# Kernel optimization log

Hardware: AMD Instinct MI355X
Metric: run time of the kernel (lower is better)

Reference implementation:

```python
import jax, jax.numpy as jnp
import numpy as np
from jax import lax

B, T, F_IN = 8, 512, 229
C1 = 48            # model_size_conv // 16
C3 = 96            # model_size_conv // 8
D_CONV = 768       # model_size_conv
D_LSTM = 768       # model_size_lstm
N_PITCH = 88       # MAX_MIDI - MIN_MIDI + 1
N_STATE = 5
EMB = 2
LSTM_IN = D_CONV + N_PITCH * EMB   # 944
FC_IN = C3 * (F_IN // 4)           # 96 * 57 = 5472
BN_EPS = 1e-5


def setup_inputs() -> dict:
    key = jax.random.key(0)
    ks = iter(jax.random.split(key, 64))
    nrm = lambda shape, s=0.05: jax.random.normal(next(ks), shape, jnp.float32) * s
    uni = lambda shape: jax.random.uniform(next(ks), shape, jnp.float32, 0.5, 1.5)
    inp = {
        'mel': jax.random.normal(next(ks), (B, T, F_IN), jnp.float32),
        'conv1_w': nrm((C1, 1, 3, 3)), 'conv1_b': nrm((C1,)),
        'bn1_g': uni((C1,)), 'bn1_b': nrm((C1,)), 'bn1_m': nrm((C1,), 0.1), 'bn1_v': uni((C1,)),
        'conv2_w': nrm((C1, C1, 3, 3)), 'conv2_b': nrm((C1,)),
        'bn2_g': uni((C1,)), 'bn2_b': nrm((C1,)), 'bn2_m': nrm((C1,), 0.1), 'bn2_v': uni((C1,)),
        'conv3_w': nrm((C3, C1, 3, 3)), 'conv3_b': nrm((C3,)),
        'bn3_g': uni((C3,)), 'bn3_b': nrm((C3,)), 'bn3_m': nrm((C3,), 0.1), 'bn3_v': uni((C3,)),
        'fc_w': nrm((D_CONV, FC_IN)), 'fc_b': nrm((D_CONV,)),
        'wih1': nrm((4 * D_LSTM, LSTM_IN)), 'whh1': nrm((4 * D_LSTM, D_LSTM)),
        'bih1': nrm((4 * D_LSTM,)), 'bhh1': nrm((4 * D_LSTM,)),
        'wih2': nrm((4 * D_LSTM, D_LSTM)), 'whh2': nrm((4 * D_LSTM, D_LSTM)),
        'bih2': nrm((4 * D_LSTM,)), 'bhh2': nrm((4 * D_LSTM,)),
        'post_w': nrm((N_PITCH * N_STATE, D_LSTM)), 'post_b': nrm((N_PITCH * N_STATE,)),
        'emb_w': nrm((N_STATE, EMB), 1.0),
    }
    return inp


def _conv_bn_relu(x, w, b, g, be, m, v):
    # x: NCHW, w: OIHW, padding 'SAME' == padding=1 for 3x3
    y = lax.conv_general_dilated(x, w, (1, 1), 'SAME', dimension_numbers=('NCHW', 'OIHW', 'NCHW'))
    y = y + b[None, :, None, None]
    scale = (g / jnp.sqrt(v + BN_EPS))[None, :, None, None]
    y = (y - m[None, :, None, None]) * scale + be[None, :, None, None]
    return jax.nn.relu(y)


def _maxpool12(x):
    # MaxPool2d((1,2)) on NCHW, floor mode
    return lax.reduce_window(x, -jnp.inf, lax.max, (1, 1, 1, 2), (1, 1, 1, 2), 'VALID')


def _lstm_cell(x, h, c, wih, whh, bih, bhh):
    z = x @ wih.T + h @ whh.T + bih + bhh
    i, f, g, o = jnp.split(z, 4, axis=-1)
    c = jax.nn.sigmoid(f) * c + jax.nn.sigmoid(i) * jnp.tanh(g)
    h = jax.nn.sigmoid(o) * jnp.tanh(c)
    return h, c


def _forward(mel, conv1_w, conv1_b, bn1_g, bn1_b, bn1_m, bn1_v,
             conv2_w, conv2_b, bn2_g, bn2_b, bn2_m, bn2_v,
             conv3_w, conv3_b, bn3_g, bn3_b, bn3_m, bn3_v,
             fc_w, fc_b, wih1, whh1, bih1, bhh1, wih2, whh2, bih2, bhh2,
             post_w, post_b, emb_w):
    b = mel.shape[0]
    # --- ConvStack acoustic model (eval mode: dropout = identity) ---
    x = mel[:, None]                                  # (B,1,T,F)
    x = _conv_bn_relu(x, conv1_w, conv1_b, bn1_g, bn1_b, bn1_m, bn1_v)
    x = _conv_bn_relu(x, conv2_w, conv2_b, bn2_g, bn2_b, bn2_m, bn2_v)
    x = _maxpool12(x)
    x = _conv_bn_relu(x, conv3_w, conv3_b, bn3_g, bn3_b, bn3_m, bn3_v)
    x = _maxpool12(x)                                 # (B,C3,T,F//4)
    x = x.transpose(0, 2, 1, 3).reshape(b, -1, FC_IN) # (B,T,C3*F//4)
    acoustic = x @ fc_w.T + fc_b                      # (B,T,768)

    def step(carry, a_t):
        h1, c1, h2, c2, prev = carry                  # prev: (B,88) int32
        emb = emb_w[prev].reshape(prev.shape[0], N_PITCH * EMB)
        xt = jnp.concatenate([a_t, emb], axis=-1)     # (B,944)
        h1n, c1n = _lstm_cell(xt, h1, c1, wih1, whh1, bih1, bhh1)
        h2n, c2n = _lstm_cell(h1n, h2, c2, wih2, whh2, bih2, bhh2)
        logits = (h2n @ post_w.T + post_b).reshape(-1, N_PITCH, N_STATE)
        nprev = jnp.argmax(logits, axis=-1).astype(jnp.int32)  # argmax(softmax)==argmax(logits)
        return (h1n, c1n, h2n, c2n, nprev), logits

    z = jnp.zeros((b, D_LSTM), mel.dtype)
    prev0 = jnp.zeros((b, N_PITCH), jnp.int32)
    _, logits = lax.scan(step, (z, z, z, z, prev0), acoustic.transpose(1, 0, 2))
    return logits.transpose(1, 0, 2, 3)               # (B,T,88,N_STATE)


def reference(mel, conv1_w, conv1_b, bn1_g, bn1_b, bn1_m, bn1_v,
              conv2_w, conv2_b, bn2_g, bn2_b, bn2_m, bn2_v,
              conv3_w, conv3_b, bn3_g, bn3_b, bn3_m, bn3_v,
              fc_w, fc_b, wih1, whh1, bih1, bhh1, wih2, whh2, bih2, bhh2,
              post_w, post_b, emb_w):
    return _forward(mel, conv1_w, conv1_b, bn1_g, bn1_b, bn1_m, bn1_v,
                    conv2_w, conv2_b, bn2_g, bn2_b, bn2_m, bn2_v,
                    conv3_w, conv3_b, bn3_g, bn3_b, bn3_m, bn3_v,
                    fc_w, fc_b, wih1, whh1, bih1, bhh1, wih2, whh2, bih2, bhh2,
                    post_w, post_b, emb_w)
```

## Files before the change

### kernel.cpp

```cpp
#include <hip/hip_runtime.h>
#include <math.h>

#define WS_C3   0u
#define WS_C2CH 22413312u
#define WS_AC   28104192u
#define WS_A1   0u
#define WS_ST   31249920u

__device__ __forceinline__ float sigm(float x){ return 1.0f / (1.0f + expf(-x)); }

__device__ __forceinline__ void cstore(float* p, float v){
  union { float f; unsigned u; } c; c.f = v;
  __hip_atomic_store((unsigned*)p, c.u, __ATOMIC_RELAXED,
                     __HIP_MEMORY_SCOPE_SYSTEM);
}
__device__ __forceinline__ void cload64(const float* p, float& a, float& b){
  unsigned long long u = __hip_atomic_load((const unsigned long long*)p,
                          __ATOMIC_RELAXED, __HIP_MEMORY_SCOPE_SYSTEM);
  union { unsigned long long u; float f[2]; } c; c.u = u;
  a = c.f[0]; b = c.f[1];
}
__device__ __forceinline__ unsigned cloadu(const unsigned* p){
  return __hip_atomic_load(p, __ATOMIC_RELAXED, __HIP_MEMORY_SCOPE_SYSTEM);
}
__device__ __forceinline__ unsigned long long cloadu64(const void* p){
  return __hip_atomic_load((const unsigned long long*)p, __ATOMIC_RELAXED,
                           __HIP_MEMORY_SCOPE_SYSTEM);
}
__device__ __forceinline__ void cstoreu64(void* p, unsigned long long v){
  __hip_atomic_store((unsigned long long*)p, v, __ATOMIC_RELAXED,
                     __HIP_MEMORY_SCOPE_SYSTEM);
}

#define SLOT 16
#define FLG  4112
#define SLOTX 8208
__device__ __forceinline__ void gbar(unsigned* sy, unsigned bar, int wg){
  __syncthreads();
  const int tid = threadIdx.x;
  if (tid == 0)
    __hip_atomic_store(&sy[SLOT + wg*16], bar, __ATOMIC_RELAXED,
                       __HIP_MEMORY_SCOPE_SYSTEM);
  if (wg == 255){
    if (tid < 64){
      for (;;){
        unsigned m0 = cloadu(&sy[SLOT + (4*tid + 0)*16]);
        unsigned m1 = cloadu(&sy[SLOT + (4*tid + 1)*16]);
        unsigned m2 = cloadu(&sy[SLOT + (4*tid + 2)*16]);
        unsigned m3 = cloadu(&sy[SLOT + (4*tid + 3)*16]);
        unsigned a = m0 < m1 ? m0 : m1;
        unsigned b = m2 < m3 ? m2 : m3;
        unsigned mn = a < b ? a : b;
        if (__all(mn >= bar)) break;
        __builtin_amdgcn_s_sleep(1);
      }
    }
    __syncthreads();
    __hip_atomic_store(&sy[FLG + tid*16], bar, __ATOMIC_RELAXED,
                       __HIP_MEMORY_SCOPE_SYSTEM);
  } else {
    if (tid == 0){
      while (cloadu(&sy[FLG + wg*16]) < bar)
        __builtin_amdgcn_s_sleep(1);
    }
  }
  __syncthreads();
}

__global__ __launch_bounds__(256) void conv2f_k(
    const float* __restrict__ mel, const float* __restrict__ w1,
    const float* __restrict__ b1, const float* __restrict__ g1,
    const float* __restrict__ be1, const float* __restrict__ m1,
    const float* __restrict__ v1,
    const float* __restrict__ w2, const float* __restrict__ b2,
    const float* __restrict__ g2, const float* __restrict__ be2,
    const float* __restrict__ m2, const float* __restrict__ v2,
    float* __restrict__ c2ch, int t0)
{
  __shared__ float act[3*8*240];
  __shared__ float w2s[48*8*12];
  __shared__ float mel5[5*240];
  __shared__ float w1s[48*12];
  __shared__ float sc1[48], sh1[48], sc2[48], sh2[48];
  int tid = threadIdx.x;
  int b = blockIdx.x / 130, lt = blockIdx.x - b*130;
  int t = t0 - 1 + lt;

  int fg = tid % 29, ocg = tid / 29;
  int f0 = fg * 8, oc0 = ocg * 6;

  if (t < 0 || t > 511){
    if (tid < 232){
      for (int o = 0; o < 6; ++o)
        for (int jj = 0; jj < 4; ++jj){
          int fp = fg*4 + jj;
          if (fp < 114)
            c2ch[((b*48 + oc0 + o)*130 + lt)*114 + fp] = 0.f;
        }
    }
    return;
  }

  for (int idx = tid; idx < 5*240; idx += 256){
    int rr = idx / 240, w = idx - rr*240;
    int tt = t + rr - 2, f = w - 2;
    mel5[idx] = (tt >= 0 && tt < 512 && f >= 0 && f < 229)
                ? mel[(b*512 + tt)*229 + f] : 0.f;
  }
  for (int idx = tid; idx < 48*12; idx += 256){
    int c = idx / 12, q = idx - c*12;
    int kh = q >> 2, kw = q & 3;
    w1s[idx] = (kw < 3) ? w1[c*9 + kh*3 + kw] : 0.f;
  }
  if (tid < 48){
    float s1 = g1[tid] / sqrtf(v1[tid] + 1e-5f);
    sc1[tid] = s1; sh1[tid] = be1[tid] + (b1[tid] - m1[tid]) * s1;
    float s2 = g2[tid] / sqrtf(v2[tid] + 1e-5f);
    sc2[tid] = s2; sh2[tid] = be2[tid] + (b2[tid] - m2[tid]) * s2;
  }

  float acc[6][8];
  #pragma unroll
  for (int o = 0; o < 6; ++o)
    #pragma unroll
    for (int j = 0; j < 8; ++j) acc[o][j] = 0.f;

  for (int ch = 0; ch < 6; ++ch){
    int ci0 = ch * 8;
    __syncthreads();
    for (int idx = tid; idx < 3*8*240; idx += 256){
      int rr = idx / 1920;
      int rem = idx - rr*1920;
      int ci = rem / 240, w = rem - ci*240;
      int tt = t + rr - 1, f = w - 1;
      float val = 0.f;
      if (tt >= 0 && tt < 512 && f >= 0 && f < 229){
        int cg = ci0 + ci;
        float a = 0.f;
        #pragma unroll
        for (int dh = 0; dh < 3; ++dh){
          const float* mr = &mel5[(rr + dh)*240 + w];
          a = fmaf(mr[0], w1s[cg*12 + dh*4 + 0], a);
          a = fmaf(mr[1], w1s[cg*12 + dh*4 + 1], a);
          a = fmaf(mr[2], w1s[cg*12 + dh*4 + 2], a);
        }
        a = a * sc1[cg] + sh1[cg];
        val = a > 0.f ? a : 0.f;
      }
      act[idx] = val;
    }
    for (int idx = tid; idx < 48*8*12; idx += 256){
      int oc = idx / 96;
      int rem = idx - oc*96;
      int ci = rem / 12, q = rem - ci*12;
      int kh = q >> 2, kw = q & 3;
      w2s[idx] = (kw < 3) ? w2[(oc*48 + ci0 + ci)*9 + kh*3 + kw] : 0.f;
    }
    __syncthreads();
    if (tid < 232){
      for (int ci = 0; ci < 8; ++ci){
        #pragma unroll
        for (int kh = 0; kh < 3; ++kh){
          const float* ap = &act[(kh*8 + ci)*240 + f0];
          float4 A0 = *(const float4*)(ap);
          float4 A1v = *(const float4*)(ap + 4);
          float4 A2 = *(const float4*)(ap + 8);
          float L[12] = {A0.x,A0.y,A0.z,A0.w,A1v.x,A1v.y,A1v.z,A1v.w,A2.x,A2.y,A2.z,A2.w};
          #pragma unroll
          for (int o = 0; o < 6; ++o){
            float4 wv = *(const float4*)&w2s[((oc0 + o)*8 + ci)*12 + kh*4];
            #pragma unroll
            for (int j = 0; j < 8; ++j)
              acc[o][j] = fmaf(L[j+2], wv.z, fmaf(L[j+1], wv.y, fmaf(L[j], wv.x, acc[o][j])));
          }
        }
      }
    }
  }
  __syncthreads();
  if (tid < 232){
    #pragma unroll
    for (int o = 0; o < 6; ++o){
      int oc = oc0 + o;
      float s = sc2[oc], hs = sh2[oc];
      #pragma unroll
      for (int jj = 0; jj < 4; ++jj){
        int fp = fg*4 + jj;
        if (fp < 114){
          float v0 = acc[o][2*jj] * s + hs;   v0 = v0 > 0.f ? v0 : 0.f;
          float v1 = acc[o][2*jj+1] * s + hs; v1 = v1 > 0.f ? v1 : 0.f;
          c2ch[((b*48 + oc)*130 + lt)*114 + fp] = v0 > v1 ? v0 : v1;
        }
      }
    }
  }
}

__global__ __launch_bounds__(256) void conv3_k(
    const float* __restrict__ c2ch, const float* __restrict__ w3,
    const float* __restrict__ b3, const float* __restrict__ g3,
    const float* __restrict__ be3, const float* __restrict__ m3,
    const float* __restrict__ v3, float* __restrict__ c3p, int t0)
{
  __shared__ float act[3*8*128];
  __shared__ float w3s[96*8*12];
  __shared__ float sc[96], sh[96];
  int tid = threadIdx.x;
  int b = blockIdx.x >> 7, tl = blockIdx.x & 127;
  int t = t0 + tl;
  if (tid < 96){
    float s = g3[tid] / sqrtf(v3[tid] + 1e-5f);
    sc[tid] = s; sh[tid] = be3[tid] + (b3[tid] - m3[tid]) * s;
  }
  int fg = tid % 15, ocg = tid / 15;
  int f0 = fg * 8, oc0 = ocg * 6;
  float acc[6][8];
  #pragma unroll
  for (int o = 0; o < 6; ++o)
    #pragma unroll
    for (int j = 0; j < 8; ++j) acc[o][j] = 0.f;

  for (int ch = 0; ch < 6; ++ch){
    int ci0 = ch * 8;
    __syncthreads();
    for (int idx = tid; idx < 3*8*128; idx += 256){
      int rr = idx >> 10;
      int rem = idx & 1023;
      int ci = rem >> 7, w = rem & 127;
      int lt = tl + rr;
      int f = w - 1;
      float val = 0.f;
      if (f >= 0 && f < 114)
        val = c2ch[((b*48 + ci0 + ci)*130 + lt)*114 + f];
      act[idx] = val;
    }
    for (int idx = tid; idx < 96*8*12; idx += 256){
      int oc = idx / 96;
      int rem = idx - oc*96;
      int ci = rem / 12, q = rem - ci*12;
      int kh = q >> 2, kw = q & 3;
      w3s[idx] = (kw < 3) ? w3[(oc*48 + ci0 + ci)*9 + kh*3 + kw] : 0.f;
    }
    __syncthreads();
    if (tid < 240){
      for (int ci = 0; ci < 8; ++ci){
        #pragma unroll
        for (int kh = 0; kh < 3; ++kh){
          const float* ap = &act[(kh*8 + ci)*128 + f0];
          float4 A0 = *(const float4*)(ap);
          float4 A1v = *(const float4*)(ap + 4);
          float4 A2 = *(const float4*)(ap + 8);
          float L[12] = {A0.x,A0.y,A0.z,A0.w,A1v.x,A1v.y,A1v.z,A1v.w,A2.x,A2.y,A2.z,A2.w};
          #pragma unroll
          for (int o = 0; o < 6; ++o){
            float4 wv = *(const float4*)&w3s[((oc0 + o)*8 + ci)*12 + kh*4];
            #pragma unroll
            for (int j = 0; j < 8; ++j)
              acc[o][j] = fmaf(L[j+2], wv.z, fmaf(L[j+1], wv.y, fmaf(L[j], wv.x, acc[o][j])));
          }
        }
      }
    }
  }
  __syncthreads();
  if (tid < 240){
    #pragma unroll
    for (int o = 0; o < 6; ++o){
      int oc = oc0 + o;
      float s = sc[oc], hs = sh[oc];
      #pragma unroll
      for (int jj = 0; jj < 4; ++jj){
        int fp = fg*4 + jj;
        if (fp < 57){
          float v0 = acc[o][2*jj] * s + hs;   v0 = v0 > 0.f ? v0 : 0.f;
          float v1 = acc[o][2*jj+1] * s + hs; v1 = v1 > 0.f ? v1 : 0.f;
          c3p[((b*96 + oc)*512 + t)*57 + fp] = v0 > v1 ? v0 : v1;
        }
      }
    }
  }
}

__global__ __launch_bounds__(256) void gemm_fc_k(
    const float* __restrict__ c3p, const float* __restrict__ fcw,
    const float* __restrict__ fcb, float* __restrict__ ac)
{
  __shared__ float As[16*132];
  __shared__ float Bs[16*132];
  int tid = threadIdx.x;
  int m0 = blockIdx.x * 128, n0 = blockIdx.y * 128;
  int tm = (tid & 15) * 8, tn = (tid >> 4) * 8;
  float acc[8][8];
  #pragma unroll
  for (int i = 0; i < 8; ++i)
    #pragma unroll
    for (int j = 0; j < 8; ++j) acc[i][j] = 0.f;

  for (int k0 = 0; k0 < 5472; k0 += 16){
    __syncthreads();
    #pragma unroll
    for (int i = 0; i < 8; ++i){
      int idx = i*256 + tid;
      int k = idx & 15, mm = idx >> 4;
      int gk = k0 + k;
      int ci = (gk * 36793) >> 21;
      int f  = gk - ci*57;
      int gm = m0 + mm;
      int bb = gm >> 9, tt = gm & 511;
      As[k*132 + mm] = c3p[((bb*96 + ci)*512 + tt)*57 + f];
      Bs[k*132 + mm] = fcw[(n0 + mm)*5472 + gk];
    }
    __syncthreads();
    #pragma unroll
    for (int k = 0; k < 16; ++k){
      const float* arow = &As[k*132 + tm];
      const float* brow = &Bs[k*132 + tn];
      float4 a0 = *(const float4*)arow, a1 = *(const float4*)(arow + 4);
      float4 b0 = *(const float4*)brow, b1 = *(const float4*)(brow + 4);
      float av[8] = {a0.x,a0.y,a0.z,a0.w,a1.x,a1.y,a1.z,a1.w};
      float bv[8] = {b0.x,b0.y,b0.z,b0.w,b1.x,b1.y,b1.z,b1.w};
      #pragma unroll
      for (int i = 0; i < 8; ++i)
        #pragma unroll
        for (int j = 0; j < 8; ++j)
          acc[i][j] = fmaf(av[i], bv[j], acc[i][j]);
    }
  }
  #pragma unroll
  for (int i = 0; i < 8; ++i){
    int gm = m0 + tm + i;
    #pragma unroll
    for (int j = 0; j < 8; ++j){
      int gn = n0 + tn + j;
      ac[gm*768 + gn] = acc[i][j] + fcb[gn];
    }
  }
}

__global__ __launch_bounds__(256) void gemm_a1_k(
    const float* __restrict__ ac, const float* __restrict__ wih1,
    const float* __restrict__ bih1, const float* __restrict__ bhh1,
    float* __restrict__ A1)
{
  __shared__ float As[16*132];
  __shared__ float Bs[16*132];
  int tid = threadIdx.x;
  int m0 = blockIdx.x * 128, n0 = blockIdx.y * 128;
  int tm = (tid & 15) * 8, tn = (tid >> 4) * 8;
  float acc[8][8];
  #pragma unroll
  for (int i = 0; i < 8; ++i)
    #pragma unroll
    for (int j = 0; j < 8; ++j) acc[i][j] = 0.f;

  for (int k0 = 0; k0 < 768; k0 += 16){
    __syncthreads();
    #pragma unroll
    for (int i = 0; i < 8; ++i){
      int idx = i*256 + tid;
      int k = idx & 15, mm = idx >> 4;
      int gk = k0 + k;
      As[k*132 + mm] = ac[(m0 + mm)*768 + gk];
      Bs[k*132 + mm] = wih1[(n0 + mm)*944 + gk];
    }
    __syncthreads();
    #pragma unroll
    for (int k = 0; k < 16; ++k){
      const float* arow = &As[k*132 + tm];
      const float* brow = &Bs[k*132 + tn];
      float4 a0 = *(const float4*)arow, a1 = *(const float4*)(arow + 4);
      float4 b0 = *(const float4*)brow, b1 = *(const float4*)(brow + 4);
      float av[8] = {a0.x,a0.y,a0.z,a0.w,a1.x,a1.y,a1.z,a1.w};
      float bv[8] = {b0.x,b0.y,b0.z,b0.w,b1.x,b1.y,b1.z,b1.w};
      #pragma unroll
      for (int i = 0; i < 8; ++i)
        #pragma unroll
        for (int j = 0; j < 8; ++j)
          acc[i][j] = fmaf(av[i], bv[j], acc[i][j]);
    }
  }
  #pragma unroll
  for (int i = 0; i < 8; ++i){
    int gm = m0 + tm + i;
    int tt = gm & 511, bb = gm >> 9;
    #pragma unroll
    for (int j = 0; j < 8; ++j){
      int gn = n0 + tn + j;
      A1[tt*24576 + gn*8 + bb] = acc[i][j] + bih1[gn] + bhh1[gn];
    }
  }
}

#define S2 772
__global__ __launch_bounds__(256, 1) void rec_k(
    const float* __restrict__ A1,
    const float* __restrict__ whh1, const float* __restrict__ wih1,
    const float* __restrict__ wih2, const float* __restrict__ whh2,
    const float* __restrict__ bih2, const float* __restrict__ bhh2,
    const float* __restrict__ postw, const float* __restrict__ postb,
    const float* __restrict__ embw,
    float* __restrict__ xbuf, float* __restrict__ h2b,
    unsigned* __restrict__ sy, float* __restrict__ out)
{
  const int wg = blockIdx.x, tid = threadIdx.x;
  const int wv = tid >> 6, l = tid & 63;
  __shared__ float xs[8*S2];
  __shared__ float h2s[8*S2];
  __shared__ float cvec[88*5*12];
  __shared__ float zbuf[96];
  __shared__ float red2[160];
  __shared__ unsigned smax[88];

  float wA[12][3];
  float wB[24][3];
  float wC[3][5];
  {
    int Rb = wv*768 + wg*3;
    #pragma unroll
    for (int ki = 0; ki < 12; ++ki){
      int k = l + (ki << 6);
      #pragma unroll
      for (int u = 0; u < 3; ++u)
        wA[ki][u] = whh1[(Rb + u)*768 + k];
    }
    #pragma unroll
    for (int ki = 0; ki < 24; ++ki){
      int k = l + (ki << 6);
      #pragma unroll
      for (int u = 0; u < 3; ++u)
        wB[ki][u] = (k < 768) ? wih2[(Rb + u)*768 + k] : whh2[(Rb + u)*768 + k - 768];
    }
  }
  if (wg < 88){
    #pragma unroll
    for (int kc = 0; kc < 3; ++kc)
      #pragma unroll
      for (int s = 0; s < 5; ++s)
        wC[kc][s] = postw[(wg*5 + s)*768 + tid + (kc << 8)];
  }
  float b2r = 0.f; int fR = 0, fb = 0;
  if (tid < 96){
    int g = tid / 24, rem = tid - g*24;
    int u = rem >> 3; fb = rem & 7;
    fR = g*768 + wg*3 + u;
    b2r = bih2[fR] + bhh2[fR];
  }
  float pbr = (wg < 88 && tid < 40) ? postb[wg*5 + (tid >> 3)] : 0.f;
  float c1r = 0.f, c2r = 0.f;

  for (int idx = tid; idx < 88*5*12; idx += 256){
    int p = idx / 60, rem = idx - p*60;
    int s = rem / 12, r = rem - s*12;
    int g = r / 3, u = r - g*3;
    int row = g*768 + wg*3 + u;
    cvec[idx] = wih1[row*944 + 768 + 2*p]     * embw[s*2]
              + wih1[row*944 + 768 + 2*p + 1] * embw[s*2 + 1];
  }
  for (int idx = tid; idx < 8*S2; idx += 256){ h2s[idx] = 0.f; xs[idx] = 0.f; }
  __syncthreads();

  unsigned bar = 0;

  for (int t = 0; t < 512; ++t){
    const int nxt = (t & 1) ^ 1;
    float* xn  = xbuf + nxt * 7552;
    float* h2n = h2b + nxt * 6144;

    float a1v = 0.f;
    if (tid < 96) a1v = A1[t*24576 + fR*8 + fb];

    {
      float acc[3][8];
      #pragma unroll
      for (int u = 0; u < 3; ++u)
        #pragma unroll
        for (int j = 0; j < 8; ++j) acc[u][j] = 0.f;
      #pragma unroll
      for (int ki = 0; ki < 12; ++ki){
        int k = l + (ki << 6);
        float x0 = xs[k],        x1 = xs[S2 + k],   x2 = xs[2*S2 + k], x3 = xs[3*S2 + k];
        float x4 = xs[4*S2 + k], x5 = xs[5*S2 + k], x6 = xs[6*S2 + k], x7 = xs[7*S2 + k];
        #pragma unroll
        for (int u = 0; u < 3; ++u){
          float w = wA[ki][u];
          acc[u][0] = fmaf(w, x0, acc[u][0]);
          acc[u][1] = fmaf(w, x1, acc[u][1]);
          acc[u][2] = fmaf(w, x2, acc[u][2]);
          acc[u][3] = fmaf(w, x3, acc[u][3]);
          acc[u][4] = fmaf(w, x4, acc[u][4]);
          acc[u][5] = fmaf(w, x5, acc[u][5]);
          acc[u][6] = fmaf(w, x6, acc[u][6]);
          acc[u][7] = fmaf(w, x7, acc[u][7]);
        }
      }
      __syncthreads();
      #pragma unroll
      for (int u = 0; u < 3; ++u)
        #pragma unroll
        for (int j = 0; j < 8; ++j){
          float s = acc[u][j];
          s += __shfl_xor(s, 1);  s += __shfl_xor(s, 2);  s += __shfl_xor(s, 4);
          s += __shfl_xor(s, 8);  s += __shfl_xor(s, 16); s += __shfl_xor(s, 32);
          if (l == 0) zbuf[wv*24 + u*8 + j] = s;
        }
      if (wv == 0){
        unsigned long long* sl = (unsigned long long*)&sy[SLOTX];
        unsigned lo0 = 0, lo1 = 0;
        for (;;){
          unsigned long long v0 = cloadu64(&sl[l*8]);
          unsigned long long v1 = 0xffffffffffffffffull;
          if (l < 24) v1 = cloadu64(&sl[(64 + l)*8]);
          unsigned t0v = (unsigned)(v0 >> 32);
          unsigned t1v = (unsigned)(v1 >> 32);
          unsigned mn = t0v < t1v ? t0v : t1v;
          if (__all(mn >= (unsigned)t)){ lo0 = (unsigned)v0; lo1 = (unsigned)v1; break; }
          __builtin_amdgcn_s_sleep(1);
        }
        smax[l] = lo0;
        if (l < 24) smax[64 + l] = lo1;
      }
      __syncthreads();
      if (tid < 96){
        int g = tid / 24;
        int rowidx = g*3 + ((tid - g*24) >> 3);
        int b = tid & 7;
        float z = zbuf[tid] + a1v;
        for (int p = 0; p < 88; ++p){
          int s = (smax[p] >> (b*4)) & 7;
          z += cvec[(p*5 + s)*12 + rowidx];
        }
        zbuf[tid] = z;
      }
      __syncthreads();
      if (tid < 24){
        float zi = zbuf[tid], zf = zbuf[24 + tid], zg = zbuf[48 + tid], zo = zbuf[72 + tid];
        c1r = sigm(zf)*c1r + sigm(zi)*tanhf(zg);
        float hh = sigm(zo)*tanhf(c1r);
        cstore(&xn[(wg*3 + (tid >> 3))*8 + (tid & 7)], hh);
      }
      ++bar; gbar(sy, bar, wg);
    }

    {
      float sa[12], sb[12];
      #pragma unroll
      for (int i = 0; i < 12; ++i){
        int idx = tid + (i << 8);
        cload64(xn + 2*idx, sa[i], sb[i]);
      }
      float acc[3][8];
      #pragma unroll
      for (int u = 0; u < 3; ++u)
        #pragma unroll
        for (int j = 0; j < 8; ++j) acc[u][j] = 0.f;
      #pragma unroll
      for (int ki = 12; ki < 24; ++ki){
        int k = l + ((ki - 12) << 6);
        float x0 = h2s[k],        x1 = h2s[S2 + k],   x2 = h2s[2*S2 + k], x3 = h2s[3*S2 + k];
        float x4 = h2s[4*S2 + k], x5 = h2s[5*S2 + k], x6 = h2s[6*S2 + k], x7 = h2s[7*S2 + k];
        #pragma unroll
        for (int u = 0; u < 3; ++u){
          float w = wB[ki][u];
          acc[u][0] = fmaf(w, x0, acc[u][0]);
          acc[u][1] = fmaf(w, x1, acc[u][1]);
          acc[u][2] = fmaf(w, x2, acc[u][2]);
          acc[u][3] = fmaf(w, x3, acc[u][3]);
          acc[u][4] = fmaf(w, x4, acc[u][4]);
          acc[u][5] = fmaf(w, x5, acc[u][5]);
          acc[u][6] = fmaf(w, x6, acc[u][6]);
          acc[u][7] = fmaf(w, x7, acc[u][7]);
        }
      }
      #pragma unroll
      for (int i = 0; i < 12; ++i){
        int idx = tid + (i << 8);
        int k = idx >> 2, p = (idx & 3) << 1;
        xs[p*S2 + k]       = sa[i];
        xs[(p + 1)*S2 + k] = sb[i];
      }
      __syncthreads();
      #pragma unroll
      for (int ki = 0; ki < 12; ++ki){
        int k = l + (ki << 6);
        float x0 = xs[k],        x1 = xs[S2 + k],   x2 = xs[2*S2 + k], x3 = xs[3*S2 + k];
        float x4 = xs[4*S2 + k], x5 = xs[5*S2 + k], x6 = xs[6*S2 + k], x7 = xs[7*S2 + k];
        #pragma unroll
        for (int u = 0; u < 3; ++u){
          float w = wB[ki][u];
          acc[u][0] = fmaf(w, x0, acc[u][0]);
          acc[u][1] = fmaf(w, x1, acc[u][1]);
          acc[u][2] = fmaf(w, x2, acc[u][2]);
          acc[u][3] = fmaf(w, x3, acc[u][3]);
          acc[u][4] = fmaf(w, x4, acc[u][4]);
          acc[u][5] = fmaf(w, x5, acc[u][5]);
          acc[u][6] = fmaf(w, x6, acc[u][6]);
          acc[u][7] = fmaf(w, x7, acc[u][7]);
        }
      }
      #pragma unroll
      for (int u = 0; u < 3; ++u)
        #pragma unroll
        for (int j = 0; j < 8; ++j){
          float s = acc[u][j];
          s += __shfl_xor(s, 1);  s += __shfl_xor(s, 2);  s += __shfl_xor(s, 4);
          s += __shfl_xor(s, 8);  s += __shfl_xor(s, 16); s += __shfl_xor(s, 32);
          if (l == 0) zbuf[wv*24 + u*8 + j] = s;
        }
      __syncthreads();
      if (tid < 96)
        zbuf[tid] += b2r;
      __syncthreads();
      if (tid < 24){
        float zi = zbuf[tid], zf = zbuf[24 + tid], zg = zbuf[48 + tid], zo = zbuf[72 + tid];
        c2r = sigm(zf)*c2r + sigm(zi)*tanhf(zg);
        float hh = sigm(zo)*tanhf(c2r);
        cstore(&h2n[(wg*3 + (tid >> 3))*8 + (tid & 7)], hh);
      }
      ++bar; gbar(sy, bar, wg);
    }

    {
      float r0[8], r1[8], r2[8];
      #pragma unroll
      for (int q = 0; q < 4; ++q){
        cload64(h2n + (tid        )*8 + 2*q, r0[2*q], r0[2*q+1]);
        cload64(h2n + (tid + 256  )*8 + 2*q, r1[2*q], r1[2*q+1]);
        cload64(h2n + (tid + 512  )*8 + 2*q, r2[2*q], r2[2*q+1]);
      }
      #pragma unroll
      for (int p = 0; p < 8; ++p){
        h2s[p*S2 + tid]       = r0[p];
        h2s[p*S2 + tid + 256] = r1[p];
        h2s[p*S2 + tid + 512] = r2[p];
      }
      if (wg < 88){
        float acc[5][8];
        #pragma unroll
        for (int s = 0; s < 5; ++s)
          #pragma unroll
          for (int j = 0; j < 8; ++j)
            acc[s][j] = fmaf(wC[2][s], r2[j],
                        fmaf(wC[1][s], r1[j], wC[0][s]*r0[j]));
        #pragma unroll
        for (int s = 0; s < 5; ++s)
          #pragma unroll
          for (int j = 0; j < 8; ++j){
            float v = acc[s][j];
            v += __shfl_xor(v, 1);  v += __shfl_xor(v, 2);  v += __shfl_xor(v, 4);
            v += __shfl_xor(v, 8);  v += __shfl_xor(v, 16); v += __shfl_xor(v, 32);
            if (l == 0) red2[(s*8 + j)*4 + wv] = v;
          }
        __syncthreads();
        if (tid < 40){
          float sum = red2[tid*4] + red2[tid*4 + 1] + red2[tid*4 + 2] + red2[tid*4 + 3] + pbr;
          int s = tid >> 3, bb = tid & 7;
          out[bb*225280 + t*440 + wg*5 + s] = sum;
          zbuf[tid] = sum;
        }
        __syncthreads();
        int bs = 0;
        if (tid < 8){
          float best = zbuf[tid];
          #pragma unroll
          for (int s = 1; s < 5; ++s){
            float v = zbuf[s*8 + tid];
            if (v > best){ best = v; bs = s; }
          }
        }
        if (wv == 0){
          unsigned lo = 0;
          #pragma unroll
          for (int b = 0; b < 8; ++b)
            lo |= (unsigned)(__shfl(bs, b) & 7) << (4*b);
          if (l == 0){
            unsigned long long pv =
                ((unsigned long long)(unsigned)(t + 1) << 32) | (unsigned long long)lo;
            cstoreu64(&sy[SLOTX + wg*16], pv);
          }
        }
      }
    }
  }
}

extern "C" void kernel_launch(void* const* d_in, const int* in_sizes, int n_in,
                              void* d_out, int out_size, void* d_ws, size_t ws_size,
                              hipStream_t stream)
{
  (void)in_sizes; (void)n_in; (void)out_size; (void)ws_size;
  const float* mel  = (const float*)d_in[0];
  const float* w1   = (const float*)d_in[1];
  const float* b1   = (const float*)d_in[2];
  const float* g1   = (const float*)d_in[3];
  const float* be1  = (const float*)d_in[4];
  const float* m1   = (const float*)d_in[5];
  const float* v1   = (const float*)d_in[6];
  const float* w2   = (const float*)d_in[7];
  const float* b2   = (const float*)d_in[8];
  const float* g2   = (const float*)d_in[9];
  const float* be2  = (const float*)d_in[10];
  const float* m2   = (const float*)d_in[11];
  const float* v2   = (const float*)d_in[12];
  const float* w3   = (const float*)d_in[13];
  const float* b3   = (const float*)d_in[14];
  const float* g3   = (const float*)d_in[15];
  const float* be3  = (const float*)d_in[16];
  const float* m3   = (const float*)d_in[17];
  const float* v3   = (const float*)d_in[18];
  const float* fcw  = (const float*)d_in[19];
  const float* fcb  = (const float*)d_in[20];
  const float* wih1 = (const float*)d_in[21];
  const float* whh1 = (const float*)d_in[22];
  const float* bih1 = (const float*)d_in[23];
  const float* bhh1 = (const float*)d_in[24];
  const float* wih2 = (const float*)d_in[25];
  const float* whh2 = (const float*)d_in[26];
  const float* bih2 = (const float*)d_in[27];
  const float* bhh2 = (const float*)d_in[28];
  const float* postw= (const float*)d_in[29];
  const float* postb= (const float*)d_in[30];
  const float* embw = (const float*)d_in[31];

  float* ws    = (float*)d_ws;
  float* c3p   = ws + WS_C3;
  float* c2ch  = ws + WS_C2CH;
  float* ac    = ws + WS_AC;
  float* A1    = ws + WS_A1;
  float* st    = ws + WS_ST;
  float* xbuf  = st;
  float* h2b   = st + 15104;
  unsigned* sy = (unsigned*)(st + 27392);
  float* outp  = (float*)d_out;

  hipMemsetAsync(st, 0, 37008 * sizeof(float), stream);

  for (int c = 0; c < 4; ++c){
    int t0 = c * 128;
    conv2f_k<<<dim3(8*130), dim3(256), 0, stream>>>(
        mel, w1, b1, g1, be1, m1, v1, w2, b2, g2, be2, m2, v2, c2ch, t0);
    conv3_k<<<dim3(8*128), dim3(256), 0, stream>>>(
        c2ch, w3, b3, g3, be3, m3, v3, c3p, t0);
  }
  gemm_fc_k<<<dim3(32, 6), dim3(256), 0, stream>>>(c3p, fcw, fcb, ac);
  gemm_a1_k<<<dim3(32, 24), dim3(256), 0, stream>>>(ac, wih1, bih1, bhh1, A1);

  rec_k<<<dim3(256), dim3(256), 0, stream>>>(
      A1, whh1, wih1, wih2, whh2, bih2, bhh2, postw, postb, embw,
      xbuf, h2b, sy, outp);
}
```

Before: 19.00 ms.

## Replace grid barriers with per-value timestep-tagged flags in LSTM recurrence

Drops the centralized grid barrier (all workgroups signal one master, which then releases them) that ran twice per timestep. Instead each hidden value is stored as a 64-bit word tagged with its timestep. Consumers spin only on the words they read, and buffers are double-buffered by timestep parity. This cuts global sync latency but doubles the bytes moved for the x/h exchange and adds per-element polling. Workspace is reused from the acoustic region and zeroed after the GEMMs.

Result: slower. 22.24 ms (+17.0%).

```diff
diff --git a/kernel.cpp b/kernel.cpp
--- a/kernel.cpp
+++ b/kernel.cpp
@@ -5,24 +5,9 @@
 #define WS_C2CH 22413312u
 #define WS_AC   28104192u
 #define WS_A1   0u
-#define WS_ST   31249920u
 
 __device__ __forceinline__ float sigm(float x){ return 1.0f / (1.0f + expf(-x)); }
 
-__device__ __forceinline__ void cstore(float* p, float v){
-  union { float f; unsigned u; } c; c.f = v;
-  __hip_atomic_store((unsigned*)p, c.u, __ATOMIC_RELAXED,
-                     __HIP_MEMORY_SCOPE_SYSTEM);
-}
-__device__ __forceinline__ void cload64(const float* p, float& a, float& b){
-  unsigned long long u = __hip_atomic_load((const unsigned long long*)p,
-                          __ATOMIC_RELAXED, __HIP_MEMORY_SCOPE_SYSTEM);
-  union { unsigned long long u; float f[2]; } c; c.u = u;
-  a = c.f[0]; b = c.f[1];
-}
-__device__ __forceinline__ unsigned cloadu(const unsigned* p){
-  return __hip_atomic_load(p, __ATOMIC_RELAXED, __HIP_MEMORY_SCOPE_SYSTEM);
-}
 __device__ __forceinline__ unsigned long long cloadu64(const void* p){
   return __hip_atomic_load((const unsigned long long*)p, __ATOMIC_RELAXED,
                            __HIP_MEMORY_SCOPE_SYSTEM);
@@ -31,40 +16,11 @@
   __hip_atomic_store((unsigned long long*)p, v, __ATOMIC_RELAXED,
                      __HIP_MEMORY_SCOPE_SYSTEM);
 }
-
-#define SLOT 16
-#define FLG  4112
-#define SLOTX 8208
-__device__ __forceinline__ void gbar(unsigned* sy, unsigned bar, int wg){
-  __syncthreads();
-  const int tid = threadIdx.x;
-  if (tid == 0)
-    __hip_atomic_store(&sy[SLOT + wg*16], bar, __ATOMIC_RELAXED,
-                       __HIP_MEMORY_SCOPE_SYSTEM);
-  if (wg == 255){
-    if (tid < 64){
-      for (;;){
-        unsigned m0 = cloadu(&sy[SLOT + (4*tid + 0)*16]);
-        unsigned m1 = cloadu(&sy[SLOT + (4*tid + 1)*16]);
-        unsigned m2 = cloadu(&sy[SLOT + (4*tid + 2)*16]);
-        unsigned m3 = cloadu(&sy[SLOT + (4*tid + 3)*16]);
-        unsigned a = m0 < m1 ? m0 : m1;
-        unsigned b = m2 < m3 ? m2 : m3;
-        unsigned mn = a < b ? a : b;
-        if (__all(mn >= bar)) break;
-        __builtin_amdgcn_s_sleep(1);
-      }
-    }
-    __syncthreads();
-    __hip_atomic_store(&sy[FLG + tid*16], bar, __ATOMIC_RELAXED,
-                       __HIP_MEMORY_SCOPE_SYSTEM);
-  } else {
-    if (tid == 0){
-      while (cloadu(&sy[FLG + wg*16]) < bar)
-        __builtin_amdgcn_s_sleep(1);
-    }
-  }
-  __syncthreads();
+__device__ __forceinline__ float u2f(unsigned u){
+  union { unsigned u; float f; } c; c.u = u; return c.f;
+}
+__device__ __forceinline__ unsigned f2u(float f){
+  union { unsigned u; float f; } c; c.f = f; return c.u;
 }
 
 __global__ __launch_bounds__(256) void conv2f_k(
@@ -399,8 +355,9 @@
     const float* __restrict__ bih2, const float* __restrict__ bhh2,
     const float* __restrict__ postw, const float* __restrict__ postb,
     const float* __restrict__ embw,
-    float* __restrict__ xbuf, float* __restrict__ h2b,
-    unsigned* __restrict__ sy, float* __restrict__ out)
+    unsigned long long* __restrict__ xat,
+    unsigned long long* __restrict__ h2at,
+    unsigned* __restrict__ slt, float* __restrict__ out)
 {
   const int wg = blockIdx.x, tid = threadIdx.x;
   const int wv = tid >> 6, l = tid & 63;
@@ -459,12 +416,10 @@
   for (int idx = tid; idx < 8*S2; idx += 256){ h2s[idx] = 0.f; xs[idx] = 0.f; }
   __syncthreads();
 
-  unsigned bar = 0;
-
   for (int t = 0; t < 512; ++t){
-    const int nxt = (t & 1) ^ 1;
-    float* xn  = xbuf + nxt * 7552;
-    float* h2n = h2b + nxt * 6144;
+    const unsigned tg = (unsigned)(t + 1);
+    unsigned long long* xb = xat  + (size_t)(t & 1) * 6144;
+    unsigned long long* hb = h2at + (size_t)(t & 1) * 6144;
 
     float a1v = 0.f;
     if (tid < 96) a1v = A1[t*24576 + fR*8 + fb];
@@ -504,7 +459,8 @@
           if (l == 0) zbuf[wv*24 + u*8 + j] = s;
         }
       if (wv == 0){
-        unsigned long long* sl = (unsigned long long*)&sy[SLOTX];
+        const unsigned long long* sl =
+            (const unsigned long long*)slt + (size_t)(t & 1) * 88 * 8;
         unsigned lo0 = 0, lo1 = 0;
         for (;;){
           unsigned long long v0 = cloadu64(&sl[l*8]);
@@ -536,18 +492,16 @@
         float zi = zbuf[tid], zf = zbuf[24 + tid], zg = zbuf[48 + tid], zo = zbuf[72 + tid];
         c1r = sigm(zf)*c1r + sigm(zi)*tanhf(zg);
         float hh = sigm(zo)*tanhf(c1r);
-        cstore(&xn[(wg*3 + (tid >> 3))*8 + (tid & 7)], hh);
-      }
-      ++bar; gbar(sy, bar, wg);
+        cstoreu64(&xb[wg*24 + tid],
+                  ((unsigned long long)tg << 32) | (unsigned long long)f2u(hh));
+      }
     }
 
     {
-      float sa[12], sb[12];
-      #pragma unroll
-      for (int i = 0; i < 12; ++i){
-        int idx = tid + (i << 8);
-        cload64(xn + 2*idx, sa[i], sb[i]);
-      }
+      unsigned long long av[24];
+      #pragma unroll
+      for (int i = 0; i < 24; ++i)
+        av[i] = cloadu64(&xb[tid + (i << 8)]);
       float acc[3][8];
       #pragma unroll
       for (int u = 0; u < 3; ++u)
@@ -571,12 +525,20 @@
           acc[u][7] = fmaf(w, x7, acc[u][7]);
         }
       }
-      #pragma unroll
-      for (int i = 0; i < 12; ++i){
+      for (;;){
+        bool bad = false;
+        #pragma unroll
+        for (int i = 0; i < 24; ++i)
+          if ((unsigned)(av[i] >> 32) < tg){
+            av[i] = cloadu64(&xb[tid + (i << 8)]); bad = true;
+          }
+        if (!__any(bad)) break;
+        __builtin_amdgcn_s_sleep(1);
+      }
+      #pragma unroll
+      for (int i = 0; i < 24; ++i){
         int idx = tid + (i << 8);
-        int k = idx >> 2, p = (idx & 3) << 1;
-        xs[p*S2 + k]       = sa[i];
-        xs[(p + 1)*S2 + k] = sb[i];
+        xs[(idx & 7)*S2 + (idx >> 3)] = u2f((unsigned)av[i]);
       }
       __syncthreads();
       #pragma unroll
@@ -614,18 +576,32 @@
         float zi = zbuf[tid], zf = zbuf[24 + tid], zg = zbuf[48 + tid], zo = zbuf[72 + tid];
         c2r = sigm(zf)*c2r + sigm(zi)*tanhf(zg);
         float hh = sigm(zo)*tanhf(c2r);
-        cstore(&h2n[(wg*3 + (tid >> 3))*8 + (tid & 7)], hh);
-      }
-      ++bar; gbar(sy, bar, wg);
+        cstoreu64(&hb[wg*24 + tid],
+                  ((unsigned long long)tg << 32) | (unsigned long long)f2u(hh));
+      }
     }
 
     {
+      unsigned long long bv[24];
+      #pragma unroll
+      for (int i = 0; i < 24; ++i)
+        bv[i] = cloadu64(&hb[(tid + ((i >> 3) << 8))*8 + (i & 7)]);
+      for (;;){
+        bool bad = false;
+        #pragma unroll
+        for (int i = 0; i < 24; ++i)
+          if ((unsigned)(bv[i] >> 32) < tg){
+            bv[i] = cloadu64(&hb[(tid + ((i >> 3) << 8))*8 + (i & 7)]); bad = true;
+          }
+        if (!__any(bad)) break;
+        __builtin_amdgcn_s_sleep(1);
+      }
       float r0[8], r1[8], r2[8];
       #pragma unroll
-      for (int q = 0; q < 4; ++q){
-        cload64(h2n + (tid        )*8 + 2*q, r0[2*q], r0[2*q+1]);
-        cload64(h2n + (tid + 256  )*8 + 2*q, r1[2*q], r1[2*q+1]);
-        cload64(h2n + (tid + 512  )*8 + 2*q, r2[2*q], r2[2*q+1]);
+      for (int q = 0; q < 8; ++q){
+        r0[q] = u2f((unsigned)bv[q]);
+        r1[q] = u2f((unsigned)bv[8 + q]);
+        r2[q] = u2f((unsigned)bv[16 + q]);
       }
       #pragma unroll
       for (int p = 0; p < 8; ++p){
@@ -674,8 +650,8 @@
             lo |= (unsigned)(__shfl(bs, b) & 7) << (4*b);
           if (l == 0){
             unsigned long long pv =
-                ((unsigned long long)(unsigned)(t + 1) << 32) | (unsigned long long)lo;
-            cstoreu64(&sy[SLOTX + wg*16], pv);
+                ((unsigned long long)tg << 32) | (unsigned long long)lo;
+            cstoreu64((unsigned long long*)slt + ((size_t)((t + 1) & 1)*88 + wg)*8, pv);
           }
         }
       }
@@ -726,13 +702,11 @@
   float* c2ch  = ws + WS_C2CH;
   float* ac    = ws + WS_AC;
   float* A1    = ws + WS_A1;
-  float* st    = ws + WS_ST;
-  float* xbuf  = st;
-  float* h2b   = st + 15104;
-  unsigned* sy = (unsigned*)(st + 27392);
+  float* st    = ws + WS_AC;
+  unsigned long long* xat  = (unsigned long long*)st;
+  unsigned long long* h2at = (unsigned long long*)(st + 24576);
+  unsigned* slt = (unsigned*)(st + 49152);
   float* outp  = (float*)d_out;
-
-  hipMemsetAsync(st, 0, 37008 * sizeof(float), stream);
 
   for (int c = 0; c < 4; ++c){
     int t0 = c * 128;
@@ -744,7 +718,9 @@
   gemm_fc_k<<<dim3(32, 6), dim3(256), 0, stream>>>(c3p, fcw, fcb, ac);
   gemm_a1_k<<<dim3(32, 24), dim3(256), 0, stream>>>(ac, wih1, bih1, bhh1, A1);
 
+  hipMemsetAsync(st, 0, 51968 * sizeof(float), stream);
+
   rec_k<<<dim3(256), dim3(256), 0, stream>>>(
       A1, whh1, wih1, wih2, whh2, bih2, bhh2, postw, postb, embw,
-      xbuf, h2b, sy, outp);
-}
+      xat, h2at, slt, outp);
+}
```

## Defer post-projection and argmax of step t-1 into the next step's layer-1 phase

Applied to the files above, without the earlier changes.

The post-linear logits and argmax for h2 of step t-1 now run at the start of step t, overlapping with the layer-1 recurrent matvec, rather than forming a separate tail phase after layer 2. The previous-state slots are double-buffered by step parity, and the final step's logits are computed after the loop. The state buffers move into the workspace region of the fc output and are zeroed after the GEMMs. This shortens the per-step critical path at the cost of more complex cross-step ordering.

Result: no change. 19.06 ms (+0.3%).

```diff
diff --git a/kernel.cpp b/kernel.cpp
--- a/kernel.cpp
+++ b/kernel.cpp
@@ -5,7 +5,6 @@
 #define WS_C2CH 22413312u
 #define WS_AC   28104192u
 #define WS_A1   0u
-#define WS_ST   31249920u
 
 __device__ __forceinline__ float sigm(float x){ return 1.0f / (1.0f + expf(-x)); }
 
@@ -34,7 +33,6 @@
 
 #define SLOT 16
 #define FLG  4112
-#define SLOTX 8208
 __device__ __forceinline__ void gbar(unsigned* sy, unsigned bar, int wg){
   __syncthreads();
   const int tid = threadIdx.x;
@@ -399,8 +397,9 @@
     const float* __restrict__ bih2, const float* __restrict__ bhh2,
     const float* __restrict__ postw, const float* __restrict__ postb,
     const float* __restrict__ embw,
-    float* __restrict__ xbuf, float* __restrict__ h2b,
-    unsigned* __restrict__ sy, float* __restrict__ out)
+    float* __restrict__ xbuf, float* __restrict__ hbuf,
+    unsigned* __restrict__ slt, unsigned* __restrict__ sy,
+    float* __restrict__ out)
 {
   const int wg = blockIdx.x, tid = threadIdx.x;
   const int wv = tid >> 6, l = tid & 63;
@@ -462,84 +461,148 @@
   unsigned bar = 0;
 
   for (int t = 0; t < 512; ++t){
-    const int nxt = (t & 1) ^ 1;
-    float* xn  = xbuf + nxt * 7552;
-    float* h2n = h2b + nxt * 6144;
+    float* xn = xbuf + (t & 1) * 6144;
+    float* hw = hbuf + (t & 1) * 6144;
+    const float* hr = hbuf + ((t ^ 1) & 1) * 6144;
 
     float a1v = 0.f;
     if (tid < 96) a1v = A1[t*24576 + fR*8 + fb];
 
-    {
-      float acc[3][8];
-      #pragma unroll
-      for (int u = 0; u < 3; ++u)
-        #pragma unroll
-        for (int j = 0; j < 8; ++j) acc[u][j] = 0.f;
-      #pragma unroll
-      for (int ki = 0; ki < 12; ++ki){
-        int k = l + (ki << 6);
-        float x0 = xs[k],        x1 = xs[S2 + k],   x2 = xs[2*S2 + k], x3 = xs[3*S2 + k];
-        float x4 = xs[4*S2 + k], x5 = xs[5*S2 + k], x6 = xs[6*S2 + k], x7 = xs[7*S2 + k];
-        #pragma unroll
-        for (int u = 0; u < 3; ++u){
-          float w = wA[ki][u];
-          acc[u][0] = fmaf(w, x0, acc[u][0]);
-          acc[u][1] = fmaf(w, x1, acc[u][1]);
-          acc[u][2] = fmaf(w, x2, acc[u][2]);
-          acc[u][3] = fmaf(w, x3, acc[u][3]);
-          acc[u][4] = fmaf(w, x4, acc[u][4]);
-          acc[u][5] = fmaf(w, x5, acc[u][5]);
-          acc[u][6] = fmaf(w, x6, acc[u][6]);
-          acc[u][7] = fmaf(w, x7, acc[u][7]);
-        }
-      }
-      __syncthreads();
-      #pragma unroll
-      for (int u = 0; u < 3; ++u)
-        #pragma unroll
-        for (int j = 0; j < 8; ++j){
-          float s = acc[u][j];
-          s += __shfl_xor(s, 1);  s += __shfl_xor(s, 2);  s += __shfl_xor(s, 4);
-          s += __shfl_xor(s, 8);  s += __shfl_xor(s, 16); s += __shfl_xor(s, 32);
-          if (l == 0) zbuf[wv*24 + u*8 + j] = s;
-        }
-      if (wv == 0){
-        unsigned long long* sl = (unsigned long long*)&sy[SLOTX];
-        unsigned lo0 = 0, lo1 = 0;
-        for (;;){
-          unsigned long long v0 = cloadu64(&sl[l*8]);
-          unsigned long long v1 = 0xffffffffffffffffull;
-          if (l < 24) v1 = cloadu64(&sl[(64 + l)*8]);
-          unsigned t0v = (unsigned)(v0 >> 32);
-          unsigned t1v = (unsigned)(v1 >> 32);
-          unsigned mn = t0v < t1v ? t0v : t1v;
-          if (__all(mn >= (unsigned)t)){ lo0 = (unsigned)v0; lo1 = (unsigned)v1; break; }
-          __builtin_amdgcn_s_sleep(1);
-        }
-        smax[l] = lo0;
-        if (l < 24) smax[64 + l] = lo1;
-      }
-      __syncthreads();
-      if (tid < 96){
-        int g = tid / 24;
-        int rowidx = g*3 + ((tid - g*24) >> 3);
-        int b = tid & 7;
-        float z = zbuf[tid] + a1v;
-        for (int p = 0; p < 88; ++p){
-          int s = (smax[p] >> (b*4)) & 7;
-          z += cvec[(p*5 + s)*12 + rowidx];
-        }
-        zbuf[tid] = z;
-      }
-      __syncthreads();
-      if (tid < 24){
-        float zi = zbuf[tid], zf = zbuf[24 + tid], zg = zbuf[48 + tid], zo = zbuf[72 + tid];
-        c1r = sigm(zf)*c1r + sigm(zi)*tanhf(zg);
-        float hh = sigm(zo)*tanhf(c1r);
-        cstore(&xn[(wg*3 + (tid >> 3))*8 + (tid & 7)], hh);
-      }
-      ++bar; gbar(sy, bar, wg);
-    }
+    float r0[8], r1[8], r2[8];
+    #pragma unroll
+    for (int q = 0; q < 8; ++q){ r0[q] = 0.f; r1[q] = 0.f; r2[q] = 0.f; }
+    if (t > 0){
+      #pragma unroll
+      for (int q = 0; q < 4; ++q){
+        cload64(hr + (tid      )*8 + 2*q, r0[2*q], r0[2*q+1]);
+        cload64(hr + (tid + 256)*8 + 2*q, r1[2*q], r1[2*q+1]);
+        cload64(hr + (tid + 512)*8 + 2*q, r2[2*q], r2[2*q+1]);
+      }
+      if (wg < 88){
+        float accL[5][8];
+        #pragma unroll
+        for (int s = 0; s < 5; ++s)
+          #pragma unroll
+          for (int j = 0; j < 8; ++j)
+            accL[s][j] = fmaf(wC[2][s], r2[j],
+                         fmaf(wC[1][s], r1[j], wC[0][s]*r0[j]));
+        #pragma unroll
+        for (int s = 0; s < 5; ++s)
+          #pragma unroll
+          for (int j = 0; j < 8; ++j){
+            float v = accL[s][j];
+            v += __shfl_xor(v, 1);  v += __shfl_xor(v, 2);  v += __shfl_xor(v, 4);
+            v += __shfl_xor(v, 8);  v += __shfl_xor(v, 16); v += __shfl_xor(v, 32);
+            if (l == 0) red2[(s*8 + j)*4 + wv] = v;
+          }
+        __syncthreads();
+        if (tid < 40){
+          float sum = red2[tid*4] + red2[tid*4 + 1] + red2[tid*4 + 2] + red2[tid*4 + 3] + pbr;
+          int s = tid >> 3, bb = tid & 7;
+          out[bb*225280 + (t-1)*440 + wg*5 + s] = sum;
+          zbuf[tid] = sum;
+        }
+        __syncthreads();
+        int bs = 0;
+        if (tid < 8){
+          float best = zbuf[tid];
+          #pragma unroll
+          for (int s = 1; s < 5; ++s){
+            float v = zbuf[s*8 + tid];
+            if (v > best){ best = v; bs = s; }
+          }
+        }
+        if (wv == 0){
+          unsigned lo = 0;
+          #pragma unroll
+          for (int b = 0; b < 8; ++b)
+            lo |= (unsigned)(__shfl(bs, b) & 7) << (4*b);
+          if (l == 0){
+            unsigned long long pv =
+                ((unsigned long long)(unsigned)t << 32) | (unsigned long long)lo;
+            cstoreu64((unsigned long long*)slt + ((size_t)(t & 1)*88 + wg)*8, pv);
+          }
+        }
+      }
+    }
+
+    float acc1[3][8];
+    #pragma unroll
+    for (int u = 0; u < 3; ++u)
+      #pragma unroll
+      for (int j = 0; j < 8; ++j) acc1[u][j] = 0.f;
+    #pragma unroll
+    for (int ki = 0; ki < 12; ++ki){
+      int k = l + (ki << 6);
+      float x0 = xs[k],        x1 = xs[S2 + k],   x2 = xs[2*S2 + k], x3 = xs[3*S2 + k];
+      float x4 = xs[4*S2 + k], x5 = xs[5*S2 + k], x6 = xs[6*S2 + k], x7 = xs[7*S2 + k];
+      #pragma unroll
+      for (int u = 0; u < 3; ++u){
+        float w = wA[ki][u];
+        acc1[u][0] = fmaf(w, x0, acc1[u][0]);
+        acc1[u][1] = fmaf(w, x1, acc1[u][1]);
+        acc1[u][2] = fmaf(w, x2, acc1[u][2]);
+        acc1[u][3] = fmaf(w, x3, acc1[u][3]);
+        acc1[u][4] = fmaf(w, x4, acc1[u][4]);
+        acc1[u][5] = fmaf(w, x5, acc1[u][5]);
+        acc1[u][6] = fmaf(w, x6, acc1[u][6]);
+        acc1[u][7] = fmaf(w, x7, acc1[u][7]);
+      }
+    }
+
+    __syncthreads();
+    #pragma unroll
+    for (int p = 0; p < 8; ++p){
+      h2s[p*S2 + tid]       = r0[p];
+      h2s[p*S2 + tid + 256] = r1[p];
+      h2s[p*S2 + tid + 512] = r2[p];
+    }
+    #pragma unroll
+    for (int u = 0; u < 3; ++u)
+      #pragma unroll
+      for (int j = 0; j < 8; ++j){
+        float s = acc1[u][j];
+        s += __shfl_xor(s, 1);  s += __shfl_xor(s, 2);  s += __shfl_xor(s, 4);
+        s += __shfl_xor(s, 8);  s += __shfl_xor(s, 16); s += __shfl_xor(s, 32);
+        if (l == 0) zbuf[wv*24 + u*8 + j] = s;
+      }
+    if (wv == 0){
+      const unsigned long long* sl =
+          (const unsigned long long*)slt + (size_t)(t & 1) * 88 * 8;
+      unsigned lo0 = 0, lo1 = 0;
+      for (;;){
+        unsigned long long v0 = cloadu64(&sl[l*8]);
+        unsigned long long v1 = 0xffffffffffffffffull;
+        if (l < 24) v1 = cloadu64(&sl[(64 + l)*8]);
+        unsigned t0v = (unsigned)(v0 >> 32);
+        unsigned t1v = (unsigned)(v1 >> 32);
+        unsigned mn = t0v < t1v ? t0v : t1v;
+        if (__all(mn >= (unsigned)t)){ lo0 = (unsigned)v0; lo1 = (unsigned)v1; break; }
+        __builtin_amdgcn_s_sleep(1);
+      }
+      smax[l] = lo0;
+      if (l < 24) smax[64 + l] = lo1;
+    }
+    __syncthreads();
+    if (tid < 96){
+      int g = tid / 24;
+      int rowidx = g*3 + ((tid - g*24) >> 3);
+      int b = tid & 7;
+      float z = zbuf[tid] + a1v;
+      for (int p = 0; p < 88; ++p){
+        int s = (smax[p] >> (b*4)) & 7;
+        z += cvec[(p*5 + s)*12 + rowidx];
+      }
+      zbuf[tid] = z;
+    }
+    __syncthreads();
+    if (tid < 24){
+      float zi = zbuf[tid], zf = zbuf[24 + tid], zg = zbuf[48 + tid], zo = zbuf[72 + tid];
+      c1r = sigm(zf)*c1r + sigm(zi)*tanhf(zg);
+      float hh = sigm(zo)*tanhf(c1r);
+      cstore(&xn[wg*24 + tid], hh);
+    }
+    ++bar; gbar(sy, bar, wg);
 
     {
       float sa[12], sb[12];
@@ -614,71 +677,42 @@
         float zi = zbuf[tid], zf = zbuf[24 + tid], zg = zbuf[48 + tid], zo = zbuf[72 + tid];
         c2r = sigm(zf)*c2r + sigm(zi)*tanhf(zg);
         float hh = sigm(zo)*tanhf(c2r);
-        cstore(&h2n[(wg*3 + (tid >> 3))*8 + (tid & 7)], hh);
+        cstore(&hw[wg*24 + tid], hh);
       }
       ++bar; gbar(sy, bar, wg);
     }
-
-    {
-      float r0[8], r1[8], r2[8];
-      #pragma unroll
-      for (int q = 0; q < 4; ++q){
-        cload64(h2n + (tid        )*8 + 2*q, r0[2*q], r0[2*q+1]);
-        cload64(h2n + (tid + 256  )*8 + 2*q, r1[2*q], r1[2*q+1]);
-        cload64(h2n + (tid + 512  )*8 + 2*q, r2[2*q], r2[2*q+1]);
-      }
-      #pragma unroll
-      for (int p = 0; p < 8; ++p){
-        h2s[p*S2 + tid]       = r0[p];
-        h2s[p*S2 + tid + 256] = r1[p];
-        h2s[p*S2 + tid + 512] = r2[p];
-      }
-      if (wg < 88){
-        float acc[5][8];
-        #pragma unroll
-        for (int s = 0; s < 5; ++s)
-          #pragma unroll
-          for (int j = 0; j < 8; ++j)
-            acc[s][j] = fmaf(wC[2][s], r2[j],
-                        fmaf(wC[1][s], r1[j], wC[0][s]*r0[j]));
-        #pragma unroll
-        for (int s = 0; s < 5; ++s)
-          #pragma unroll
-          for (int j = 0; j < 8; ++j){
-            float v = acc[s][j];
-            v += __shfl_xor(v, 1);  v += __shfl_xor(v, 2);  v += __shfl_xor(v, 4);
-            v += __shfl_xor(v, 8);  v += __shfl_xor(v, 16); v += __shfl_xor(v, 32);
-            if (l == 0) red2[(s*8 + j)*4 + wv] = v;
-          }
-        __syncthreads();
-        if (tid < 40){
-          float sum = red2[tid*4] + red2[tid*4 + 1] + red2[tid*4 + 2] + red2[tid*4 + 3] + pbr;
-          int s = tid >> 3, bb = tid & 7;
-          out[bb*225280 + t*440 + wg*5 + s] = sum;
-          zbuf[tid] = sum;
-        }
-        __syncthreads();
-        int bs = 0;
-        if (tid < 8){
-          float best = zbuf[tid];
-          #pragma unroll
-          for (int s = 1; s < 5; ++s){
-            float v = zbuf[s*8 + tid];
-            if (v > best){ best = v; bs = s; }
-          }
-        }
-        if (wv == 0){
-          unsigned lo = 0;
-          #pragma unroll
-          for (int b = 0; b < 8; ++b)
-            lo |= (unsigned)(__shfl(bs, b) & 7) << (4*b);
-          if (l == 0){
-            unsigned long long pv =
-                ((unsigned long long)(unsigned)(t + 1) << 32) | (unsigned long long)lo;
-            cstoreu64(&sy[SLOTX + wg*16], pv);
-          }
-        }
-      }
+  }
+
+  if (wg < 88){
+    const float* hr = hbuf + 6144;
+    float r0[8], r1[8], r2[8];
+    #pragma unroll
+    for (int q = 0; q < 4; ++q){
+      cload64(hr + (tid      )*8 + 2*q, r0[2*q], r0[2*q+1]);
+      cload64(hr + (tid + 256)*8 + 2*q, r1[2*q], r1[2*q+1]);
+      cload64(hr + (tid + 512)*8 + 2*q, r2[2*q], r2[2*q+1]);
+    }
+    float accL[5][8];
+    #pragma unroll
+    for (int s = 0; s < 5; ++s)
+      #pragma unroll
+      for (int j = 0; j < 8; ++j)
+        accL[s][j] = fmaf(wC[2][s], r2[j],
+                     fmaf(wC[1][s], r1[j], wC[0][s]*r0[j]));
+    #pragma unroll
+    for (int s = 0; s < 5; ++s)
+      #pragma unroll
+      for (int j = 0; j < 8; ++j){
+        float v = accL[s][j];
+        v += __shfl_xor(v, 1);  v += __shfl_xor(v, 2);  v += __shfl_xor(v, 4);
+        v += __shfl_xor(v, 8);  v += __shfl_xor(v, 16); v += __shfl_xor(v, 32);
+        if (l == 0) red2[(s*8 + j)*4 + wv] = v;
+      }
+    __syncthreads();
+    if (tid < 40){
+      float sum = red2[tid*4] + red2[tid*4 + 1] + red2[tid*4 + 2] + red2[tid*4 + 3] + pbr;
+      int s = tid >> 3, bb = tid & 7;
+      out[bb*225280 + 511*440 + wg*5 + s] = sum;
     }
   }
 }
@@ -726,13 +760,12 @@
   float* c2ch  = ws + WS_C2CH;
   float* ac    = ws + WS_AC;
   float* A1    = ws + WS_A1;
-  float* st    = ws + WS_ST;
+  float* st    = ws + WS_AC;
   float* xbuf  = st;
-  float* h2b   = st + 15104;
-  unsigned* sy = (unsigned*)(st + 27392);
+  float* hbuf  = st + 12288;
+  unsigned* slt = (unsigned*)(st + 24576);
+  unsigned* sy  = (unsigned*)(st + 27392);
   float* outp  = (float*)d_out;
-
-  hipMemsetAsync(st, 0, 37008 * sizeof(float), stream);
 
   for (int c = 0; c < 4; ++c){
     int t0 = c * 128;
@@ -744,7 +777,9 @@
   gemm_fc_k<<<dim3(32, 6), dim3(256), 0, stream>>>(c3p, fcw, fcb, ac);
   gemm_a1_k<<<dim3(32, 24), dim3(256), 0, stream>>>(ac, wih1, bih1, bhh1, A1);
 
+  hipMemsetAsync(st, 0, 35600 * sizeof(float), stream);
+
   rec_k<<<dim3(256), dim3(256), 0, stream>>>(
       A1, whh1, wih1, wih2, whh2, bih2, bhh2, postw, postb, embw,
-      xbuf, h2b, sy, outp);
-}
+      xbuf, hbuf, slt, sy, outp);
+}
```
